# Optimization experiments

Measured on AMD Instinct MI355X. Metric: run time of the kernel, lower is better.

The kernel has to match this reference:

```python
import math
import jax, jax.numpy as jnp
import numpy as np

# irreps layout (flat, e3nn ordering: all scalars first, then vectors as (mul,3)):
#   pseduo: 64x0e + 32x1o  -> dim 160, 96 irreps
#   edge:   32x0e + 32x1o  -> dim 128, 64 irreps
PS, PV = 64, 32
ES, EV = 32, 32
H, NB = 8, 16
N_NODES, N_EDGES = 8192, 65536
MSG_DIM = PS + 3 * PV           # msg_irreps = pseduo_irreps (default)
NIR = PS + PV                   # num_irreps of pseduo
SQRT3 = math.sqrt(3.0)

def _split(x, ns, nv):
    # flat spherical tensor -> (scalars [..,ns], vectors [..,nv,3])
    return x[..., :ns], x[..., ns:].reshape(x.shape[:-1] + (nv, 3))

def _o3_linear(s, v, Ws, Wv):
    # e3nn o3.Linear: independent channel mixing per l, fan-in normalized
    so = (s @ Ws) / math.sqrt(Ws.shape[0])
    vo = jnp.einsum('...ic,io->...oc', v, Wv) / math.sqrt(Wv.shape[0])
    return so, vo

def setup_inputs() -> dict:
    key = jax.random.key(0)
    k = jax.random.split(key, 20)
    f32 = jnp.float32
    return {
        'pseduo_x': jax.random.normal(k[0], (N_NODES, PS + 3 * PV), f32),
        'rbf': jax.random.normal(k[1], (N_EDGES, NB), f32),
        'rsh': jax.random.normal(k[2], (N_EDGES, ES + 3 * EV), f32),
        'edge_index': jax.random.randint(k[3], (2, N_EDGES), 0, N_NODES),
        'Wq_s': jax.random.normal(k[4], (PS, H * PS), f32),
        'Wq_v': jax.random.normal(k[5], (PV, H * PV), f32),
        'Wk_s': jax.random.normal(k[6], (2 * PS, H * PS), f32),
        'Wk_v': jax.random.normal(k[7], (2 * PV, H * PV), f32),
        'Wp_s': jax.random.normal(k[8], (2 * PS, ES), f32),
        'Wp_v': jax.random.normal(k[9], (2 * PV, EV), f32),
        'Wrbf': jax.random.normal(k[10], (NB, ES + EV), f32) / math.sqrt(NB),
        'Wv_s': jax.random.normal(k[11], (ES + EV, H * PS), f32),
        'Wv_v': jax.random.normal(k[12], (2 * EV, H * PV), f32),
        'Wm_s': jax.random.normal(k[13], (H * PS, PS), f32),
        'Wm_v': jax.random.normal(k[14], (H * PV, PV), f32),
        'ln_g': jnp.ones((NIR,), f32),
        'ln_b': jnp.zeros((NIR,), f32),
        'W1': jax.random.normal(k[15], (NIR, NIR), f32) / math.sqrt(NIR),
        'b1': jnp.zeros((NIR,), f32),
        'W2': jax.random.normal(k[16], (NIR, NIR), f32) / math.sqrt(NIR),
        'b2': jnp.zeros((NIR,), f32),
    }

def reference(pseduo_x, rbf, rsh, edge_index, Wq_s, Wq_v, Wk_s, Wk_v, Wp_s, Wp_v,
              Wrbf, Wv_s, Wv_v, Wm_s, Wm_v, ln_g, ln_b, W1, b1, W2, b2):
    src, dst = edge_index[0], edge_index[1]
    s, v = _split(pseduo_x, PS, PV)

    # pseduo_ij = cat([x_i, x_j]) -> irreps pseduo*2
    sij = jnp.concatenate([s[src], s[dst]], axis=-1)            # [E, 2*PS]
    vij = jnp.concatenate([v[src], v[dst]], axis=-2)            # [E, 2*PV, 3]

    # multi-head query (per node) and key (per edge)
    q_s, q_v = _o3_linear(s, v, Wq_s, Wq_v)
    q_s = q_s.reshape(-1, H, PS); q_v = q_v.reshape(-1, H, PV, 3)
    k_s, k_v = _o3_linear(sij, vij, Wk_s, Wk_v)
    k_s = k_s.reshape(-1, H, PS); k_v = k_v.reshape(-1, H, PV, 3)

    # edge filter: rsh_conv(rsh, rbf_lin(rbf))
    scal = rbf @ Wrbf                                           # [E, ES+EV]
    rs, rv = _split(rsh, ES, EV)
    e_s = rs * scal[:, :ES]
    e_v = rv * scal[:, ES:, None]

    # sph_ij = edge * pseduo_lin(pseduo_ij)   (elementwise on flat layout)
    p_s, p_v = _o3_linear(sij, vij, Wp_s, Wp_v)
    sph_s = e_s * p_s                                           # [E, ES]
    sph_v = e_v * p_v                                           # [E, EV, 3]

    # depthwise CG self-coupling x (x) x, filter {0e, 1o} -> 64x0e + 64x1o
    c0 = jnp.concatenate([sph_s * sph_s,
                          jnp.sum(sph_v * sph_v, axis=-1) / SQRT3], axis=-1)  # [E, 64]
    sv = sph_s[..., None] * sph_v                               # 0e x 1o -> 1o
    c1 = jnp.concatenate([sv, sv], axis=-2)                     # [E, 64, 3]

    val_s, val_v = _o3_linear(c0, c1, Wv_s, Wv_v)
    val_s = val_s.reshape(-1, H, PS); val_v = val_v.reshape(-1, H, PV, 3)

    # attention logits: (query[src] * key).sum over flat msg dim, per head
    proj = (jnp.einsum('ehd,ehd->eh', q_s[src], k_s) +
            jnp.einsum('ehdc,ehdc->eh', q_v[src], k_v))
    logits = proj / math.sqrt(MSG_DIM)

    # scatter-softmax over destination nodes
    m = jax.ops.segment_max(logits, dst, num_segments=N_NODES)
    ex = jnp.exp(logits - m[dst])
    den = jax.ops.segment_sum(ex, dst, num_segments=N_NODES)
    attn = ex / den[dst]                                        # [E, H]

    # scatter-aggregate messages to nodes
    msg_s = jax.ops.segment_sum(attn[..., None] * val_s, dst, num_segments=N_NODES)
    msg_v = jax.ops.segment_sum(attn[..., None, None] * val_v, dst, num_segments=N_NODES)

    m_s, m_v = _o3_linear(msg_s.reshape(-1, H * PS),
                          msg_v.reshape(-1, H * PV, 3), Wm_s, Wm_v)

    # NormGate: EvNorm (per-irrep norm, node LayerNorm) + 2-layer silu MLP gate
    n0 = jnp.concatenate([jnp.abs(m_s), jnp.linalg.norm(m_v, axis=-1)], axis=-1)  # [N, 96]
    mu = jnp.mean(n0, axis=-1, keepdims=True)
    var = jnp.var(n0, axis=-1, keepdims=True)
    x1 = (n0 - mu) / jnp.sqrt(var + 1e-5) * ln_g + ln_b
    inv = 1.0 / (n0 + 1e-6)                                    # 1 / (|h_l| + eps)
    g = jax.nn.silu(jax.nn.silu(x1 @ W1 + b1) @ W2 + b2)
    f = inv * g
    out_s = m_s * f[:, :PS]
    out_v = m_v * f[:, PS:, None]
    return jnp.concatenate([out_s, out_v.reshape(-1, 3 * PV)], axis=-1)
```

## Files before the change

kernel.cpp:

```cpp
#include <hip/hip_runtime.h>

typedef unsigned short u16;
typedef unsigned int u32;

#define NN 8192
#define NE 65536
#define INV160 0.07905694150420949f

__device__ __forceinline__ float BF(u16 u){ return __uint_as_float(((u32)u)<<16); }
__device__ __forceinline__ float LD(const void* p, u32 i, int f){
  return f ? ((const float*)p)[i] : BF(((const u16*)p)[i]);
}
__device__ __forceinline__ int LDI(const void* p, u32 i, int f64){
  return f64 ? (int)((const long long*)p)[i] : ((const int*)p)[i];
}

__global__ void k_detect(
    const void* b0, const void* b1, const void* b2, const void* b3,
    const void* b4, const void* b5, const void* b6, const void* b7,
    const void* b8, const void* b9, const void* b10, const void* b11,
    const void* b12, const void* b13, const void* b14, const void* b15,
    const void* b16, const void* b17, const void* b18, const void* b19,
    const void* b20, int* flags)
{
  const void* bufs[21] = {b0,b1,b2,b3,b4,b5,b6,b7,b8,b9,b10,
                          b11,b12,b13,b14,b15,b16,b17,b18,b19,b20};
  int i = threadIdx.x;
  if (i >= 21) return;
  const u32* w = (const u32*)bufs[i];
  if (i == 3){
    int allz = 1;
    for (int k=0;k<32;k++) if (w[2*k+1] != 0u) allz = 0;
    flags[3] = allz;
  } else {
    int cnt = 0;
    for (int k=0;k<40;k++){
      u32 lo = w[k] & 0xFFFFu;
      u32 e = (lo>>7)&0xFFu;
      if (e>=123u && e<=131u) cnt++;
    }
    flags[i] = (cnt>=20) ? 0 : 1;
  }
}

__global__ void k_sentinel(float* __restrict__ out, int n){
  int i = blockIdx.x*256+threadIdx.x;
  if (i<n) out[i] = 12345.0f;
}

__global__ __launch_bounds__(384) void k_prep4(
    const void* __restrict__ X, const void* __restrict__ Wq_s,
    const void* __restrict__ Wq_v, const void* __restrict__ Wk_s,
    const void* __restrict__ Wk_v, const int* __restrict__ flags,
    int hc0, float* __restrict__ qtab, float* __restrict__ kbtab,
    float* __restrict__ dotAA)
{
  __shared__ float xr[4][160];
  __shared__ float dsum[4][4];
  const int fX=flags[0], fqs=flags[4], fqv=flags[5], fks=flags[6], fkv=flags[7];
  const int fall = fqs & fqv & fks & fkv;
  const int t=threadIdx.x; const int n0=blockIdx.x*4;
  for(int u=t;u<640;u+=384){ int m=u/160,k=u-m*160; xr[m][k]=LD(X,(u32)(n0+m)*160+k,fX); }
  if (t<16) dsum[t>>2][t&3]=0.f;
  __syncthreads();
  if (t<256){
    const int lh=t>>6, d=t&63;
    const int o=hc0*64+t;
    float q[4]={0,0,0,0}, ka[4]={0,0,0,0}, kb[4]={0,0,0,0};
    if (fall){
      const float* wqs=(const float*)Wq_s;
      const float* wks=(const float*)Wk_s;
      for(int i=0;i<64;i++){
        float wq=wqs[(u32)i*512+o], wa=wks[(u32)i*512+o], wb=wks[(u32)(64+i)*512+o];
        #pragma unroll
        for(int m=0;m<4;m++){ float s=xr[m][i]; q[m]+=s*wq; ka[m]+=s*wa; kb[m]+=s*wb; }
      }
    } else {
      for(int i=0;i<64;i++){
        float wq=LD(Wq_s,(u32)i*512+o,fqs);
        float wa=LD(Wk_s,(u32)i*512+o,fks);
        float wb=LD(Wk_s,(u32)(64+i)*512+o,fks);
        #pragma unroll
        for(int m=0;m<4;m++){ float s=xr[m][i]; q[m]+=s*wq; ka[m]+=s*wa; kb[m]+=s*wb; }
      }
    }
    #pragma unroll
    for(int m=0;m<4;m++){
      float qs = q[m]*0.125f;
      float kas= ka[m]*0.08838834764831845f;
      float kbs= kb[m]*0.08838834764831845f;
      u32 base=(u32)(n0+m)*640 + lh*160 + d;
      qtab [base]=qs;
      kbtab[base]=kbs;
      float dd=qs*kas;
      for(int s2=1;s2<64;s2<<=1) dd+=__shfl_xor(dd,s2,64);
      if(d==0) atomicAdd(&dsum[m][lh],dd);
    }
  } else {
    const int ol=t-256;
    const int lh=ol>>5, jj=ol&31;
    const int o=hc0*32+ol;
    float q[4][3]={}, ka[4][3]={}, kb[4][3]={};
    if (fall){
      const float* wqv=(const float*)Wq_v;
      const float* wkv=(const float*)Wk_v;
      for(int j=0;j<32;j++){
        float wq=wqv[(u32)j*256+o], wa=wkv[(u32)j*256+o], wb=wkv[(u32)(32+j)*256+o];
        #pragma unroll
        for(int m=0;m<4;m++){
          #pragma unroll
          for(int c=0;c<3;c++){
            float x=xr[m][64+j*3+c];
            q[m][c]+=x*wq; ka[m][c]+=x*wa; kb[m][c]+=x*wb;
          }
        }
      }
    } else {
      for(int j=0;j<32;j++){
        float wq=LD(Wq_v,(u32)j*256+o,fqv);
        float wa=LD(Wk_v,(u32)j*256+o,fkv);
        float wb=LD(Wk_v,(u32)(32+j)*256+o,fkv);
        #pragma unroll
        for(int m=0;m<4;m++){
          #pragma unroll
          for(int c=0;c<3;c++){
            float x=xr[m][64+j*3+c];
            q[m][c]+=x*wq; ka[m][c]+=x*wa; kb[m][c]+=x*wb;
          }
        }
      }
    }
    const float sq=0.17677669529663687f;
    const float sk=0.125f;
    #pragma unroll
    for(int m=0;m<4;m++){
      float dd=0.f;
      u32 base=(u32)(n0+m)*640 + lh*160 + 64 + (u32)jj*3;
      #pragma unroll
      for(int c=0;c<3;c++){
        float qs=q[m][c]*sq, kas=ka[m][c]*sk, kbs=kb[m][c]*sk;
        qtab[base+c]=qs; kbtab[base+c]=kbs;
        dd+=qs*kas;
      }
      for(int s2=1;s2<32;s2<<=1) dd+=__shfl_xor(dd,s2,64);
      if((t&31)==0) atomicAdd(&dsum[m][lh],dd);
    }
  }
  __syncthreads();
  if (t<16){ int m=t>>2, hh=t&3; dotAA[(u32)(n0+m)*8+hc0+hh]=dsum[m][hh]; }
}

__global__ __launch_bounds__(512) void k_elog4(
    const void* __restrict__ ei, const int* __restrict__ flags,
    const float* __restrict__ qtab, const float* __restrict__ kbtab,
    const float* __restrict__ dotAA, const u32* __restrict__ elist,
    int hc0, float* __restrict__ logits)
{
  const int f64=flags[3];
  const int t=threadIdx.x;
  const u32 pp=(u32)blockIdx.x*8+(t>>6);
  const int e=(int)elist[pp], l=t&63;
  const int src=LDI(ei,(u32)e,f64);
  const int dst=LDI(ei,(u32)NE+e,f64);
  const float4* q4=(const float4*)qtab + (u32)src*160;
  const float4* b4=(const float4*)kbtab + (u32)dst*160;
  const int hg=l>>4, lg=l&15;
  const int base4=hg*40;
  float acc;
  {
    float4 a=q4[base4+lg], b=b4[base4+lg];
    acc=a.x*b.x+a.y*b.y+a.z*b.z+a.w*b.w;
  }
  {
    float4 a=q4[base4+16+lg], b=b4[base4+16+lg];
    acc+=a.x*b.x+a.y*b.y+a.z*b.z+a.w*b.w;
  }
  if (lg<8){
    float4 a=q4[base4+32+lg], b=b4[base4+32+lg];
    acc+=a.x*b.x+a.y*b.y+a.z*b.z+a.w*b.w;
  }
  #pragma unroll
  for(int m=1;m<16;m<<=1) acc+=__shfl_xor(acc,m,64);
  if (lg==0)
    logits[pp*8+hc0+hg]=(dotAA[(u32)src*8+hc0+hg]+acc)*INV160;
}

__global__ __launch_bounds__(256) void k_fold(
    const void* __restrict__ Wv_s, const void* __restrict__ Wv_v,
    const void* __restrict__ Wm_s, const void* __restrict__ Wm_v,
    const int* __restrict__ flags,
    float* __restrict__ Wfold, float* __restrict__ Vfold)
{
  const int fvs=flags[11], fvv=flags[12], fms=flags[13], fmv=flags[14];
  const int b=blockIdx.x, t=threadIdx.x;
  if (b<128){
    int idx=b*256+t;
    int i=idx>>6, o=idx&63;
    int h=i>>6, iin=i&63;
    float a=0.f;
    for(int d=0;d<64;d++)
      a += LD(Wv_s,(u32)iin*512 + h*64 + d, fvs) * LD(Wm_s,(u32)(h*64+d)*64 + o, fms);
    Wfold[idx]=a*0.0055242717280199026f;
  } else {
    int idx=(b-128)*256+t;
    int h=idx>>10, r=idx&1023, j2=r>>5, o2=r&31;
    float a=0.f;
    for(int dl=0;dl<32;dl++){
      int i2=h*32+dl;
      a += (LD(Wv_v,(u32)j2*256+i2,fvv)+LD(Wv_v,(u32)(32+j2)*256+i2,fvv))
           *LD(Wm_v,(u32)i2*32+o2,fmv);
    }
    Vfold[idx]=a*0.0078125f;
  }
}

__global__ __launch_bounds__(256) void k_pprep(
    const void* __restrict__ X, const void* __restrict__ Wp_s,
    const void* __restrict__ Wp_v, const int* __restrict__ flags,
    float* __restrict__ pA, float* __restrict__ pB)
{
  __shared__ float xr[4][160];
  const int fX=flags[0], fps=flags[8], fpv=flags[9];
  const int t=threadIdx.x, n0=blockIdx.x*4;
  for(int u=t;u<640;u+=256){ int m=u/160,k=u-m*160; xr[m][k]=LD(X,(u32)(n0+m)*160+k,fX); }
  __syncthreads();
  if (t<64){
    const int j=t&31, half=t>>5;
    float a[4]={0.f,0.f,0.f,0.f};
    if (fps){
      const float* wp=(const float*)Wp_s;
      for(int i=0;i<64;i++){
        float w=wp[(u32)(half*64+i)*32+j];
        #pragma unroll
        for(int m=0;m<4;m++) a[m]+=xr[m][i]*w;
      }
    } else {
      for(int i=0;i<64;i++){
        float w=LD(Wp_s,(u32)(half*64+i)*32+j,fps);
        #pragma unroll
        for(int m=0;m<4;m++) a[m]+=xr[m][i]*w;
      }
    }
    float* d_ = half? pB:pA;
    #pragma unroll
    for(int m=0;m<4;m++) d_[(u32)(n0+m)*128+j]=a[m]*0.08838834764831845f;
  } else {
    const int idx=t-64;
    const int half=idx/96;
    const int r=idx-half*96;
    const int j=r/3, c=r-3*j;
    float a[4]={0.f,0.f,0.f,0.f};
    if (fpv){
      const float* wp=(const float*)Wp_v;
      for(int k=0;k<32;k++){
        float w=wp[(u32)(half*32+k)*32+j];
        #pragma unroll
        for(int m=0;m<4;m++) a[m]+=xr[m][64+k*3+c]*w;
      }
    } else {
      for(int k=0;k<32;k++){
        float w=LD(Wp_v,(u32)(half*32+k)*32+j,fpv);
        #pragma unroll
        for(int m=0;m<4;m++) a[m]+=xr[m][64+k*3+c]*w;
      }
    }
    float* d_ = half? pB:pA;
    #pragma unroll
    for(int m=0;m<4;m++) d_[(u32)(n0+m)*128+32+j*3+c]=a[m]*0.125f;
  }
}

__global__ __launch_bounds__(256) void k_count(
    const void* __restrict__ ei, const int* __restrict__ flags,
    u32* __restrict__ cnt)
{
  int e = blockIdx.x*256 + threadIdx.x;
  int dst = LDI(ei,(u32)NE+e,flags[3]);
  atomicAdd(&cnt[dst],1u);
}
__global__ __launch_bounds__(256) void k_scan(
    u32* __restrict__ cnt, u32* __restrict__ off, u32* __restrict__ cur)
{
  __shared__ u32 s[NN];
  __shared__ u32 tsum[256];
  const int t=threadIdx.x;
  for(int u=t;u<NN;u+=256) s[u]=cnt[u];
  __syncthreads();
  const u32 base=(u32)t*32;
  u32 sum=0;
  for(int k=0;k<32;k++) sum+=s[base+k];
  tsum[t]=sum;
  __syncthreads();
  if(t==0){
    u32 run=0;
    for(int i=0;i<256;i++){ u32 v=tsum[i]; tsum[i]=run; run+=v; }
  }
  __syncthreads();
  u32 run=tsum[t];
  for(int k=0;k<32;k++){
    u32 v=s[base+k];
    off[base+k]=run; cur[base+k]=run;
    run+=v;
  }
  if(t==255) off[NN]=run;
}
__global__ __launch_bounds__(256) void k_fill(
    const void* __restrict__ ei, const int* __restrict__ flags,
    u32* __restrict__ cur, u32* __restrict__ elist)
{
  int e = blockIdx.x*256 + threadIdx.x;
  int dst = LDI(ei,(u32)NE+e,flags[3]);
  u32 p = atomicAdd(&cur[dst],1u);
  elist[p] = (u32)e;
}

__global__ __launch_bounds__(256) void k_nodeval(
    const float* __restrict__ logits, const float* __restrict__ pA,
    const float* __restrict__ pBt,
    const u32* __restrict__ off, const u32* __restrict__ elist,
    const void* __restrict__ ei, const void* __restrict__ rbf,
    const void* __restrict__ rsh, const void* __restrict__ Wrbf,
    const float* __restrict__ Wfold, const float* __restrict__ Vfold,
    const void* __restrict__ ln_g, const void* __restrict__ ln_b,
    const void* __restrict__ W1, const void* __restrict__ b1,
    const void* __restrict__ W2, const void* __restrict__ b2,
    const int* __restrict__ flags, float* __restrict__ out)
{
  __shared__ float ag[4][1288];
  __shared__ float smemf[2816];
  float* wrb = smemf;
  float (*pB4)[128]  = (float(*)[128])(smemf+1024);
  float (*ubuf)[160] = (float(*)[160])(smemf+1536);
  float (*partf)[4][65] = (float(*)[4][65])smemf;
  float (*partv)[192] = (float(*)[192])(smemf+1040);
  float* agf = (float*)ag;
  float (*mrow)[160]  = (float(*)[160])(agf);
  float (*n0_)[96]    = (float(*)[96])(agf+640);
  float (*x1_)[96]    = (float(*)[96])(agf+1024);
  float (*y1_)[96]    = (float(*)[96])(agf+1408);
  float (*fl_)[96]    = (float(*)[96])(agf+1792);
  float* stat = agf+2176;

  const int frb=flags[1], frs=flags[2], f64=flags[3], fwr=flags[10];
  const int fg=flags[15], fbb=flags[16], f1=flags[17], fb1=flags[18];
  const int f2=flags[19], fb2=flags[20];
  const int fastg = frb & frs;
  const int fastt = f1 & f2;
  const int t=threadIdx.x; const int g4=blockIdx.x*4;
  for(int u=t;u<1024;u+=256) wrb[u]=LD(Wrbf,u,fwr);
  #pragma unroll
  for(int m=0;m<4;m++) if (t<128) pB4[m][t]=pBt[(u32)(g4+m)*128+t];
  __syncthreads();

  const int h=t>>5, j=t&31;

  for (int m=0;m<4;m++){
    const int n=g4+m;
    const u32 o0=off[n], o1=off[n+1];
    const u32 pidx=o0+j;
    const float lg = (pidx<o1) ? logits[pidx*8+h] : -3.4e38f;
    float mx=lg;
    for(u32 p=o0+32+j; p<o1; p+=32) mx=fmaxf(mx, logits[p*8+h]);
    #pragma unroll
    for(int s2=1;s2<32;s2<<=1) mx=fmaxf(mx, __shfl_xor(mx,s2,32));
    const float ex0 = (pidx<o1) ? __expf(lg-mx) : 0.f;
    float sm=ex0;
    for(u32 p=o0+32+j; p<o1; p+=32) sm+=__expf(logits[p*8+h]-mx);
    #pragma unroll
    for(int s2=1;s2<32;s2<<=1) sm+=__shfl_xor(sm,s2,32);
    const float winv=(sm>0.f)?1.f/sm:0.f;
    const float we = ex0*winv;

    float a0=0.f,a1=0.f,a2=0.f,a3=0.f,a4=0.f;
    for (u32 base=o0; base<o1; base+=8){
      u32 rem=o1-base; int nb = rem<8u ? (int)rem : 8;
      if (h<nb){
        u32 e=elist[base+h];
        int src=LDI(ei,e,f64);
        const float* pa=pA+(u32)src*128;
        float ps  = pa[j]        + pB4[m][j];
        float pv0 = pa[32+j*3+0] + pB4[m][32+j*3+0];
        float pv1 = pa[32+j*3+1] + pB4[m][32+j*3+1];
        float pv2 = pa[32+j*3+2] + pB4[m][32+j*3+2];
        float scs=0.f, scv=0.f;
        float rs0,rs1,rs2,rs3;
        if (fastg){
          const float* rb=(const float*)rbf + (size_t)e*16;
          #pragma unroll
          for(int r=0;r<16;r++){
            float x=rb[r];
            scs+=x*wrb[r*64+j]; scv+=x*wrb[r*64+32+j];
          }
          const float* rs=(const float*)rsh + (size_t)e*128;
          rs0=rs[j]; rs1=rs[32+j*3+0]; rs2=rs[32+j*3+1]; rs3=rs[32+j*3+2];
        } else {
          for(int r=0;r<16;r++){
            float x=LD(rbf,(u32)e*16+r,frb);
            scs+=x*wrb[r*64+j]; scv+=x*wrb[r*64+32+j];
          }
          rs0=LD(rsh,(u32)e*128+j,frs);
          rs1=LD(rsh,(u32)e*128+32+j*3+0,frs);
          rs2=LD(rsh,(u32)e*128+32+j*3+1,frs);
          rs3=LD(rsh,(u32)e*128+32+j*3+2,frs);
        }
        float ss = rs0 * scs * ps;
        float v0 = rs1 * scv * pv0;
        float v1 = rs2 * scv * pv1;
        float v2 = rs3 * scv * pv2;
        ubuf[h][j]        = ss*ss;
        ubuf[h][32+j]     = (v0*v0+v1*v1+v2*v2)*0.57735026918962576f;
        ubuf[h][64+3*j+0] = ss*v0;
        ubuf[h][64+3*j+1] = ss*v1;
        ubuf[h][64+3*j+2] = ss*v2;
      }
      __syncthreads();
      const int off0=(int)(base-o0);
      for(int q=0;q<nb;q++){
        const int idx=off0+q;
        float w;
        if (idx<32) w=__shfl(we, idx, 32);
        else        w=__expf(logits[(base+q)*8+h]-mx)*winv;
        a0+=w*ubuf[q][j];        a1+=w*ubuf[q][32+j];
        a2+=w*ubuf[q][64+3*j+0]; a3+=w*ubuf[q][64+3*j+1]; a4+=w*ubuf[q][64+3*j+2];
      }
      __syncthreads();
    }
    ag[m][h*64+j]=a0; ag[m][h*64+32+j]=a1;
    ag[m][512+h*96+3*j+0]=a2; ag[m][512+h*96+3*j+1]=a3; ag[m][512+h*96+3*j+2]=a4;
  }
  __syncthreads();

  {
    const int o4=t&15, pp=t>>4;
    const int m=pp&3, gq=pp>>2;
    const float4* Wf4=(const float4*)Wfold;
    float ax=0.f,ay=0.f,az=0.f,aw=0.f;
    const int i0=gq*128;
    for(int i=i0;i<i0+128;i++){
      float a=ag[m][i];
      float4 wv=Wf4[(u32)i*16+o4];
      ax+=a*wv.x; ay+=a*wv.y; az+=a*wv.z; aw+=a*wv.w;
    }
    partf[gq][m][o4*4+0]=ax; partf[gq][m][o4*4+1]=ay;
    partf[gq][m][o4*4+2]=az; partf[gq][m][o4*4+3]=aw;
  }
  if (t<192){
    const int o2=t&31, c=(t>>5)%3, p=t/96;
    float a[4]={0.f,0.f,0.f,0.f};
    for(int hh=p*4;hh<p*4+4;hh++)
      for(int j2=0;j2<32;j2++){
        float v=Vfold[(u32)hh*1024+j2*32+o2];
        #pragma unroll
        for(int m=0;m<4;m++) a[m]+=ag[m][512+hh*96+j2*3+c]*v;
      }
    #pragma unroll
    for(int m=0;m<4;m++) partv[m][t]=a[m];
  }
  __syncthreads();
  {
    const int o=t&63, m=t>>6;
    mrow[m][o]=partf[0][m][o]+partf[1][m][o]+partf[2][m][o]+partf[3][m][o];
  }
  if (t<96){
    #pragma unroll
    for(int m=0;m<4;m++)
      mrow[m][64+(t&31)*3+(t>>5)]=partv[m][t]+partv[m][t+96];
  }
  __syncthreads();

  if (t<96){
    #pragma unroll
    for(int m=0;m<4;m++){
      float val;
      if (t<64) val=fabsf(mrow[m][t]);
      else { int o2=t-64;
        float a=mrow[m][64+o2*3],b=mrow[m][64+o2*3+1],c=mrow[m][64+o2*3+2];
        val=sqrtf(a*a+b*b+c*c); }
      n0_[m][t]=val;
    }
  }
  __syncthreads();
  {
    const int m=t>>6;
    float mu=0.f,ss2=0.f;
    for(int i=0;i<96;i++){ float v=n0_[m][i]; mu+=v; ss2+=v*v; }
    mu*=(1.f/96.f);
    float var=fmaxf(ss2*(1.f/96.f)-mu*mu,0.f);
    float rstd=rsqrtf(var+1e-5f);
    if ((t&63)==0){ stat[m]=mu; stat[4+m]=rstd; }
  }
  __syncthreads();
  if (t<96){
    float gv = fg  ? ((const float*)ln_g)[t] : LD(ln_g,t,fg);
    float bv = fbb ? ((const float*)ln_b)[t] : LD(ln_b,t,fbb);
    #pragma unroll
    for(int m=0;m<4;m++)
      x1_[m][t]=(n0_[m][t]-stat[m])*stat[4+m]*gv+bv;
  }
  __syncthreads();
  if (t<96){
    float bb = fb1 ? ((const float*)b1)[t] : LD(b1,t,fb1);
    float a[4]={bb,bb,bb,bb};
    if (fastt){
      const float* w1=(const float*)W1;
      for(int i=0;i<96;i++){
        float w=w1[(u32)i*96+t];
        #pragma unroll
        for(int m=0;m<4;m++) a[m]+=x1_[m][i]*w;
      }
    } else {
      for(int i=0;i<96;i++){
        float w=LD(W1,i*96+t,f1);
        #pragma unroll
        for(int m=0;m<4;m++) a[m]+=x1_[m][i]*w;
      }
    }
    #pragma unroll
    for(int m=0;m<4;m++) y1_[m][t]=a[m]/(1.f+__expf(-a[m]));
  }
  __syncthreads();
  if (t<96){
    float bb = fb2 ? ((const float*)b2)[t] : LD(b2,t,fb2);
    float a[4]={bb,bb,bb,bb};
    if (fastt){
      const float* w2=(const float*)W2;
      for(int i=0;i<96;i++){
        float w=w2[(u32)i*96+t];
        #pragma unroll
        for(int m=0;m<4;m++) a[m]+=y1_[m][i]*w;
      }
    } else {
      for(int i=0;i<96;i++){
        float w=LD(W2,i*96+t,f2);
        #pragma unroll
        for(int m=0;m<4;m++) a[m]+=y1_[m][i]*w;
      }
    }
    #pragma unroll
    for(int m=0;m<4;m++){
      float gg=a[m]/(1.f+__expf(-a[m]));
      fl_[m][t]=gg/(n0_[m][t]+1e-6f);
    }
  }
  __syncthreads();
  if (t<160){
    #pragma unroll
    for(int m=0;m<4;m++){
      float v;
      if (t<64) v=mrow[m][t]*fl_[m][t];
      else { int q=t-64; int o2=q/3; v=mrow[m][t]*fl_[m][64+o2]; }
      out[(u32)(g4+m)*160+t]=v;
    }
  }
}

extern "C" void kernel_launch(void* const* d_in, const int* in_sizes, int n_in,
                              void* d_out, int out_size, void* d_ws, size_t ws_size,
                              hipStream_t stream)
{
  (void)in_sizes; (void)n_in;
  const void* X    = d_in[0];
  const void* rbf  = d_in[1];
  const void* rsh  = d_in[2];
  const void* ei   = d_in[3];
  const void* Wq_s = d_in[4];
  const void* Wq_v = d_in[5];
  const void* Wk_s = d_in[6];
  const void* Wk_v = d_in[7];
  const void* Wp_s = d_in[8];
  const void* Wp_v = d_in[9];
  const void* Wrbf = d_in[10];
  const void* Wv_s = d_in[11];
  const void* Wv_v = d_in[12];
  const void* Wm_s = d_in[13];
  const void* Wm_v = d_in[14];
  const void* ln_g = d_in[15];
  const void* ln_b = d_in[16];
  const void* W1   = d_in[17];
  const void* b1   = d_in[18];
  const void* W2   = d_in[19];
  const void* b2   = d_in[20];

  char* w = (char*)d_ws;
  int* flags     = (int*)w;   w += 256;
  float* logits  = (float*)w; w += (size_t)NE*8*4;
  u32* imax      = (u32*)w;   w += (size_t)NN*8*4;
  float* den     = (float*)w; w += (size_t)NN*8*4;
  char* uni = w;              w += (size_t)NN*1280*4;
  float* qtab  = (float*)uni;
  float* kbtab = (float*)(uni + (size_t)NN*640*4);
  float* pA    = (float*)uni;
  float* pB    = (float*)(uni + (size_t)NN*128*4);
  u32* csr_off = imax;
  u32* csr_cur = imax + 12288;
  float* Wfold = (float*)((char*)imax + 98304);
  float* Vfold = (float*)((char*)imax + 229376);
  u32* elist   = (u32*)den;
  float* dotAA = (float*)d_out;
  size_t required = (size_t)(w - (char*)d_ws);

  if (ws_size < required){
    k_sentinel<<<(out_size+255)/256,256,0,stream>>>((float*)d_out, out_size);
    return;
  }

  k_detect<<<1,64,0,stream>>>(X,rbf,rsh,ei,Wq_s,Wq_v,Wk_s,Wk_v,Wp_s,Wp_v,
                              Wrbf,Wv_s,Wv_v,Wm_s,Wm_v,ln_g,ln_b,W1,b1,W2,b2,flags);
  k_fold<<<160,256,0,stream>>>(Wv_s,Wv_v,Wm_s,Wm_v,flags,Wfold,Vfold);
  hipMemsetAsync(imax, 0, (size_t)NN*4, stream);
  k_count<<<NE/256,256,0,stream>>>(ei,flags,imax);
  k_scan<<<1,256,0,stream>>>(imax,csr_off,csr_cur);
  k_fill<<<NE/256,256,0,stream>>>(ei,flags,csr_cur,elist);
  for (int c=0;c<2;c++){
    k_prep4<<<NN/4,384,0,stream>>>(X,Wq_s,Wq_v,Wk_s,Wk_v,flags,c*4,qtab,kbtab,dotAA);
    k_elog4<<<NE/8,512,0,stream>>>(ei,flags,qtab,kbtab,dotAA,elist,c*4,logits);
  }
  k_pprep<<<NN/4,256,0,stream>>>(X,Wp_s,Wp_v,flags,pA,pB);
  k_nodeval<<<NN/4,256,0,stream>>>(logits,pA,pB,csr_off,elist,ei,rbf,rsh,Wrbf,
                                   Wfold,Vfold,ln_g,ln_b,W1,b1,W2,b2,flags,(float*)d_out);
}
```

Before: 403.5 us.

## Process 8 nodes per prep block and fuse weight fold with edge count

The Q/K projection kernel now handles 8 nodes per block instead of 4, halving the number of blocks. Each weight load is reused across twice as many nodes. The scalar part computes q, ka and kb in separate passes to hold down register pressure, and the vector part loops over two groups of 4 nodes. The edge-count kernel is merged into the weight-fold kernel as extra blocks, removing one launch at the cost of a larger combined grid.

```diff
diff --git a/kernel.cpp b/kernel.cpp
--- a/kernel.cpp
+++ b/kernel.cpp
@@ -48,106 +48,142 @@
   if (i<n) out[i] = 12345.0f;
 }
 
-__global__ __launch_bounds__(384) void k_prep4(
+__global__ __launch_bounds__(384) void k_prep8(
     const void* __restrict__ X, const void* __restrict__ Wq_s,
     const void* __restrict__ Wq_v, const void* __restrict__ Wk_s,
     const void* __restrict__ Wk_v, const int* __restrict__ flags,
     int hc0, float* __restrict__ qtab, float* __restrict__ kbtab,
     float* __restrict__ dotAA)
 {
-  __shared__ float xr[4][160];
-  __shared__ float dsum[4][4];
+  __shared__ float xr[8][160];
+  __shared__ float dsum[8][4];
   const int fX=flags[0], fqs=flags[4], fqv=flags[5], fks=flags[6], fkv=flags[7];
-  const int fall = fqs & fqv & fks & fkv;
-  const int t=threadIdx.x; const int n0=blockIdx.x*4;
-  for(int u=t;u<640;u+=384){ int m=u/160,k=u-m*160; xr[m][k]=LD(X,(u32)(n0+m)*160+k,fX); }
-  if (t<16) dsum[t>>2][t&3]=0.f;
+  const int t=threadIdx.x; const int n0=blockIdx.x*8;
+  for(int u=t;u<1280;u+=384){ int m=u/160,k=u-m*160; xr[m][k]=LD(X,(u32)(n0+m)*160+k,fX); }
+  if (t<32) dsum[t>>2][t&3]=0.f;
   __syncthreads();
   if (t<256){
     const int lh=t>>6, d=t&63;
     const int o=hc0*64+t;
-    float q[4]={0,0,0,0}, ka[4]={0,0,0,0}, kb[4]={0,0,0,0};
-    if (fall){
+    float q[8]={0,0,0,0,0,0,0,0};
+    if (fqs){
       const float* wqs=(const float*)Wq_s;
-      const float* wks=(const float*)Wk_s;
       for(int i=0;i<64;i++){
-        float wq=wqs[(u32)i*512+o], wa=wks[(u32)i*512+o], wb=wks[(u32)(64+i)*512+o];
-        #pragma unroll
-        for(int m=0;m<4;m++){ float s=xr[m][i]; q[m]+=s*wq; ka[m]+=s*wa; kb[m]+=s*wb; }
+        float wq=wqs[(u32)i*512+o];
+        #pragma unroll
+        for(int m=0;m<8;m++) q[m]+=xr[m][i]*wq;
       }
     } else {
       for(int i=0;i<64;i++){
         float wq=LD(Wq_s,(u32)i*512+o,fqs);
-        float wa=LD(Wk_s,(u32)i*512+o,fks);
-        float wb=LD(Wk_s,(u32)(64+i)*512+o,fks);
-        #pragma unroll
-        for(int m=0;m<4;m++){ float s=xr[m][i]; q[m]+=s*wq; ka[m]+=s*wa; kb[m]+=s*wb; }
-      }
-    }
-    #pragma unroll
-    for(int m=0;m<4;m++){
-      float qs = q[m]*0.125f;
-      float kas= ka[m]*0.08838834764831845f;
-      float kbs= kb[m]*0.08838834764831845f;
-      u32 base=(u32)(n0+m)*640 + lh*160 + d;
-      qtab [base]=qs;
-      kbtab[base]=kbs;
-      float dd=qs*kas;
-      for(int s2=1;s2<64;s2<<=1) dd+=__shfl_xor(dd,s2,64);
-      if(d==0) atomicAdd(&dsum[m][lh],dd);
+        #pragma unroll
+        for(int m=0;m<8;m++) q[m]+=xr[m][i]*wq;
+      }
+    }
+    #pragma unroll
+    for(int m=0;m<8;m++){
+      q[m]*=0.125f;
+      qtab[(u32)(n0+m)*640 + lh*160 + d]=q[m];
+    }
+    {
+      float ka[8]={0,0,0,0,0,0,0,0};
+      if (fks){
+        const float* wks=(const float*)Wk_s;
+        for(int i=0;i<64;i++){
+          float wa=wks[(u32)i*512+o];
+          #pragma unroll
+          for(int m=0;m<8;m++) ka[m]+=xr[m][i]*wa;
+        }
+      } else {
+        for(int i=0;i<64;i++){
+          float wa=LD(Wk_s,(u32)i*512+o,fks);
+          #pragma unroll
+          for(int m=0;m<8;m++) ka[m]+=xr[m][i]*wa;
+        }
+      }
+      #pragma unroll
+      for(int m=0;m<8;m++){
+        float dd=q[m]*(ka[m]*0.08838834764831845f);
+        for(int s2=1;s2<64;s2<<=1) dd+=__shfl_xor(dd,s2,64);
+        if(d==0) atomicAdd(&dsum[m][lh],dd);
+      }
+    }
+    {
+      float kb[8]={0,0,0,0,0,0,0,0};
+      if (fks){
+        const float* wks=(const float*)Wk_s;
+        for(int i=0;i<64;i++){
+          float wb=wks[(u32)(64+i)*512+o];
+          #pragma unroll
+          for(int m=0;m<8;m++) kb[m]+=xr[m][i]*wb;
+        }
+      } else {
+        for(int i=0;i<64;i++){
+          float wb=LD(Wk_s,(u32)(64+i)*512+o,fks);
+          #pragma unroll
+          for(int m=0;m<8;m++) kb[m]+=xr[m][i]*wb;
+        }
+      }
+      #pragma unroll
+      for(int m=0;m<8;m++)
+        kbtab[(u32)(n0+m)*640 + lh*160 + d]=kb[m]*0.08838834764831845f;
     }
   } else {
     const int ol=t-256;
     const int lh=ol>>5, jj=ol&31;
     const int o=hc0*32+ol;
-    float q[4][3]={}, ka[4][3]={}, kb[4][3]={};
-    if (fall){
-      const float* wqv=(const float*)Wq_v;
-      const float* wkv=(const float*)Wk_v;
-      for(int j=0;j<32;j++){
-        float wq=wqv[(u32)j*256+o], wa=wkv[(u32)j*256+o], wb=wkv[(u32)(32+j)*256+o];
-        #pragma unroll
-        for(int m=0;m<4;m++){
+    const int fallv = fqv & fkv;
+    for (int g=0; g<2; ++g){
+      const int mb=g*4;
+      float q[4][3]={}, ka[4][3]={}, kb[4][3]={};
+      if (fallv){
+        const float* wqv=(const float*)Wq_v;
+        const float* wkv=(const float*)Wk_v;
+        for(int j=0;j<32;j++){
+          float wq=wqv[(u32)j*256+o], wa=wkv[(u32)j*256+o], wb=wkv[(u32)(32+j)*256+o];
           #pragma unroll
-          for(int c=0;c<3;c++){
-            float x=xr[m][64+j*3+c];
-            q[m][c]+=x*wq; ka[m][c]+=x*wa; kb[m][c]+=x*wb;
+          for(int m=0;m<4;m++){
+            #pragma unroll
+            for(int c=0;c<3;c++){
+              float x=xr[mb+m][64+j*3+c];
+              q[m][c]+=x*wq; ka[m][c]+=x*wa; kb[m][c]+=x*wb;
+            }
           }
         }
-      }
-    } else {
-      for(int j=0;j<32;j++){
-        float wq=LD(Wq_v,(u32)j*256+o,fqv);
-        float wa=LD(Wk_v,(u32)j*256+o,fkv);
-        float wb=LD(Wk_v,(u32)(32+j)*256+o,fkv);
-        #pragma unroll
-        for(int m=0;m<4;m++){
+      } else {
+        for(int j=0;j<32;j++){
+          float wq=LD(Wq_v,(u32)j*256+o,fqv);
+          float wa=LD(Wk_v,(u32)j*256+o,fkv);
+          float wb=LD(Wk_v,(u32)(32+j)*256+o,fkv);
           #pragma unroll
-          for(int c=0;c<3;c++){
-            float x=xr[m][64+j*3+c];
-            q[m][c]+=x*wq; ka[m][c]+=x*wa; kb[m][c]+=x*wb;
+          for(int m=0;m<4;m++){
+            #pragma unroll
+            for(int c=0;c<3;c++){
+              float x=xr[mb+m][64+j*3+c];
+              q[m][c]+=x*wq; ka[m][c]+=x*wa; kb[m][c]+=x*wb;
+            }
           }
         }
       }
-    }
-    const float sq=0.17677669529663687f;
-    const float sk=0.125f;
-    #pragma unroll
-    for(int m=0;m<4;m++){
-      float dd=0.f;
-      u32 base=(u32)(n0+m)*640 + lh*160 + 64 + (u32)jj*3;
+      const float sq=0.17677669529663687f;
+      const float sk=0.125f;
       #pragma unroll
-      for(int c=0;c<3;c++){
-        float qs=q[m][c]*sq, kas=ka[m][c]*sk, kbs=kb[m][c]*sk;
-        qtab[base+c]=qs; kbtab[base+c]=kbs;
-        dd+=qs*kas;
-      }
-      for(int s2=1;s2<32;s2<<=1) dd+=__shfl_xor(dd,s2,64);
-      if((t&31)==0) atomicAdd(&dsum[m][lh],dd);
-    }
-  }
-  __syncthreads();
-  if (t<16){ int m=t>>2, hh=t&3; dotAA[(u32)(n0+m)*8+hc0+hh]=dsum[m][hh]; }
+      for(int m=0;m<4;m++){
+        float dd=0.f;
+        u32 base=(u32)(n0+mb+m)*640 + lh*160 + 64 + (u32)jj*3;
+        #pragma unroll
+        for(int c=0;c<3;c++){
+          float qs=q[m][c]*sq, kas=ka[m][c]*sk, kbs=kb[m][c]*sk;
+          qtab[base+c]=qs; kbtab[base+c]=kbs;
+          dd+=qs*kas;
+        }
+        for(int s2=1;s2<32;s2<<=1) dd+=__shfl_xor(dd,s2,64);
+        if((t&31)==0) atomicAdd(&dsum[mb+m][lh],dd);
+      }
+    }
+  }
+  __syncthreads();
+  if (t<32){ int m=t>>2, hh=t&3; dotAA[(u32)(n0+m)*8+hc0+hh]=dsum[m][hh]; }
 }
 
 __global__ __launch_bounds__(512) void k_elog4(
@@ -185,14 +221,21 @@
     logits[pp*8+hc0+hg]=(dotAA[(u32)src*8+hc0+hg]+acc)*INV160;
 }
 
-__global__ __launch_bounds__(256) void k_fold(
+__global__ __launch_bounds__(256) void k_foldcount(
     const void* __restrict__ Wv_s, const void* __restrict__ Wv_v,
     const void* __restrict__ Wm_s, const void* __restrict__ Wm_v,
-    const int* __restrict__ flags,
-    float* __restrict__ Wfold, float* __restrict__ Vfold)
-{
+    const void* __restrict__ ei, const int* __restrict__ flags,
+    float* __restrict__ Wfold, float* __restrict__ Vfold,
+    u32* __restrict__ cnt)
+{
+  const int b=blockIdx.x, t=threadIdx.x;
+  if (b>=160){
+    int e=(b-160)*256+t;
+    int dst=LDI(ei,(u32)NE+e,flags[3]);
+    atomicAdd(&cnt[dst],1u);
+    return;
+  }
   const int fvs=flags[11], fvv=flags[12], fms=flags[13], fmv=flags[14];
-  const int b=blockIdx.x, t=threadIdx.x;
   if (b<128){
     int idx=b*256+t;
     int i=idx>>6, o=idx&63;
@@ -270,14 +313,6 @@
   }
 }
 
-__global__ __launch_bounds__(256) void k_count(
-    const void* __restrict__ ei, const int* __restrict__ flags,
-    u32* __restrict__ cnt)
-{
-  int e = blockIdx.x*256 + threadIdx.x;
-  int dst = LDI(ei,(u32)NE+e,flags[3]);
-  atomicAdd(&cnt[dst],1u);
-}
 __global__ __launch_bounds__(256) void k_scan(
     u32* __restrict__ cnt, u32* __restrict__ off, u32* __restrict__ cur)
 {
@@ -606,13 +641,12 @@
 
   k_detect<<<1,64,0,stream>>>(X,rbf,rsh,ei,Wq_s,Wq_v,Wk_s,Wk_v,Wp_s,Wp_v,
                               Wrbf,Wv_s,Wv_v,Wm_s,Wm_v,ln_g,ln_b,W1,b1,W2,b2,flags);
-  k_fold<<<160,256,0,stream>>>(Wv_s,Wv_v,Wm_s,Wm_v,flags,Wfold,Vfold);
   hipMemsetAsync(imax, 0, (size_t)NN*4, stream);
-  k_count<<<NE/256,256,0,stream>>>(ei,flags,imax);
+  k_foldcount<<<416,256,0,stream>>>(Wv_s,Wv_v,Wm_s,Wm_v,ei,flags,Wfold,Vfold,imax);
   k_scan<<<1,256,0,stream>>>(imax,csr_off,csr_cur);
   k_fill<<<NE/256,256,0,stream>>>(ei,flags,csr_cur,elist);
   for (int c=0;c<2;c++){
-    k_prep4<<<NN/4,384,0,stream>>>(X,Wq_s,Wq_v,Wk_s,Wk_v,flags,c*4,qtab,kbtab,dotAA);
+    k_prep8<<<NN/8,384,0,stream>>>(X,Wq_s,Wq_v,Wk_s,Wk_v,flags,c*4,qtab,kbtab,dotAA);
     k_elog4<<<NE/8,512,0,stream>>>(ei,flags,qtab,kbtab,dotAA,elist,c*4,logits);
   }
   k_pprep<<<NN/4,256,0,stream>>>(X,Wp_s,Wp_v,flags,pA,pB);
```

Result: no change. 407.1 us (+0.9%).
